# Performance work log

Measured on AMD Instinct MI355X. Metric: run time of the kernel, lower is better.

Reference implementation:

```python
import jax, jax.numpy as jnp
import numpy as np

B, T, TQ, E = 32, 200, 50, 64
P, C = 128, 64
BN_EPS = 1e-6
DICE_EPS = 1e-6


def _bn(x, g, b, m, v):
    # inference-mode batch norm over last axis
    return (x - m) * jax.lax.rsqrt(v + BN_EPS) * g + b


def _dice(x, alpha, m, v):
    # Dice activation: p = sigmoid(BN(x, no scale/shift)); out = p*x + alpha*(1-p)*x
    p = jax.nn.sigmoid((x - m) * jax.lax.rsqrt(v + DICE_EPS))
    return p * x + alpha * (1.0 - p) * x


def setup_inputs() -> dict:
    key = jax.random.key(0)
    ks = jax.random.split(key, 16)
    def g(k, shape, scale=0.05):
        return jax.random.normal(k, shape, dtype=jnp.float32) * scale
    inp = {
        "user_behavior": jax.random.normal(ks[0], (B, T, E), dtype=jnp.float32),
        "items": jax.random.normal(ks[1], (B, TQ, E), dtype=jnp.float32),
        "user_profile": jax.random.normal(ks[2], (B, P), dtype=jnp.float32),
        "context": jax.random.normal(ks[3], (B, C), dtype=jnp.float32),
        # attention MLP
        "W1": g(ks[4], (4 * E, 36)), "b1": jnp.zeros((36,), jnp.float32),
        "dice_alpha": jnp.zeros((36,), jnp.float32),
        "dice_mean": jnp.zeros((36,), jnp.float32),
        "dice_var": jnp.ones((36,), jnp.float32),
        "W2": g(ks[5], (36, 1)), "b2": jnp.zeros((1,), jnp.float32),
        # trunk MLP (input dim E+P+C = 256)
        "bn1_g": jnp.ones((E + P + C,), jnp.float32), "bn1_b": jnp.zeros((E + P + C,), jnp.float32),
        "bn1_m": jnp.zeros((E + P + C,), jnp.float32), "bn1_v": jnp.ones((E + P + C,), jnp.float32),
        "Wm1": g(ks[6], (E + P + C, 256)), "bm1": jnp.zeros((256,), jnp.float32),
        "bn2_g": jnp.ones((256,), jnp.float32), "bn2_b": jnp.zeros((256,), jnp.float32),
        "bn2_m": jnp.zeros((256,), jnp.float32), "bn2_v": jnp.ones((256,), jnp.float32),
        "Wm2": g(ks[7], (256, 128)), "bm2": jnp.zeros((128,), jnp.float32),
        "bn3_g": jnp.ones((128,), jnp.float32), "bn3_b": jnp.zeros((128,), jnp.float32),
        "bn3_m": jnp.zeros((128,), jnp.float32), "bn3_v": jnp.ones((128,), jnp.float32),
        "Wm3": g(ks[8], (128, 64)), "bm3": jnp.zeros((64,), jnp.float32),
    }
    return inp


def reference(user_behavior, items, user_profile, context,
              W1, b1, dice_alpha, dice_mean, dice_var, W2, b2,
              bn1_g, bn1_b, bn1_m, bn1_v, Wm1, bm1,
              bn2_g, bn2_b, bn2_m, bn2_v, Wm2, bm2,
              bn3_g, bn3_b, bn3_m, bn3_v, Wm3, bm3):
    b, t, e = user_behavior.shape
    tq = items.shape[1]
    # tile/concat cross product: (B, T', T, 4E)
    q = jnp.broadcast_to(user_behavior[:, None, :, :], (b, tq, t, e))
    k = jnp.broadcast_to(items[:, :, None, :], (b, tq, t, e))
    x = jnp.concatenate([q, k, q - k, q * k], axis=-1)
    x = jnp.einsum('btsf,fu->btsu', x, W1) + b1
    x = _dice(x, dice_alpha, dice_mean, dice_var)
    weight = (jnp.einsum('btsu,uo->btso', x, W2) + b2)[..., 0]  # (B, T', T)
    # weighted sum over history: (B, T', E)
    interest = jnp.einsum('bts,bse->bte', weight, user_behavior)
    # trunk MLP (dropout is identity at inference)
    up = jnp.broadcast_to(user_profile[:, None, :], (b, tq, user_profile.shape[-1]))
    cx = jnp.broadcast_to(context[:, None, :], (b, tq, context.shape[-1]))
    h = jnp.concatenate([interest, up, cx], axis=-1)
    h = _bn(h, bn1_g, bn1_b, bn1_m, bn1_v)
    h = jax.nn.relu(h @ Wm1 + bm1)
    h = _bn(h, bn2_g, bn2_b, bn2_m, bn2_v)
    h = jax.nn.relu(h @ Wm2 + bm2)
    h = _bn(h, bn3_g, bn3_b, bn3_m, bn3_v)
    h = jax.nn.relu(h @ Wm3 + bm3)
    return h
```

## Files before the change

kernel.cpp:

```cpp
#include <hip/hip_runtime.h>
#include <hip/hip_bf16.h>
#include <math.h>

#define NB  32
#define NT  200
#define NTQ 50
#define NE  64
#define NP  128
#define NC  64
#define NU  36
#define NROW (NB * NTQ)

typedef __attribute__((ext_vector_type(8))) short bf8;
typedef __attribute__((ext_vector_type(4))) float f4;

#define KW_F32   0
#define BF_BASE  57600
#define W1F_OFF  0
#define WM1F_OFF 6144
#define WM2F_OFF 71680
#define WM3F_OFF 104448
#define HH_OFF   112640

__device__ __forceinline__ short f2bf(float x) {
    __hip_bfloat16 h = __float2bfloat16(x);
    return __builtin_bit_cast(short, h);
}

__device__ __forceinline__ void pack_frag(int j, const float* W, int N, int ksc, short* dst) {
    int i    = j & 7;
    int lane = (j >> 3) & 63;
    int tile = j >> 9;
    int ks = tile % ksc;
    int nt = tile / ksc;
    int k = ks * 32 + 8 * (lane >> 4) + i;
    int n = nt * 16 + (lane & 15);
    dst[j] = f2bf(W[k * N + n]);
}

__global__ __launch_bounds__(256) void prep(
    const float* __restrict__ it,
    const float* __restrict__ up, const float* __restrict__ cx,
    const float* __restrict__ W1, const float* __restrict__ b1,
    const float* __restrict__ Wm1, const float* __restrict__ Wm2, const float* __restrict__ Wm3,
    const float* __restrict__ bn1_g, const float* __restrict__ bn1_b,
    const float* __restrict__ bn1_m, const float* __restrict__ bn1_v,
    float* __restrict__ kW,
    short* __restrict__ w1f, short* __restrict__ wm1f,
    short* __restrict__ wm2f, short* __restrict__ wm3f, short* __restrict__ Hh)
{
    int idx = blockIdx.x * 256 + threadIdx.x;
    if (idx < NB * NTQ * NU) {
        int u = idx % NU, row = idx / NU;
        const float* k = it + row * NE;
        float acc = b1[u];
        #pragma unroll 4
        for (int e = 0; e < NE; ++e)
            acc = fmaf(k[e], W1[(64 + e) * NU + u] - W1[(128 + e) * NU + u], acc);
        kW[idx] = acc;
        return;
    }
    idx -= NB * NTQ * NU;
    if (idx < 6144) {
        int i = idx & 7, lane = (idx >> 3) & 63, tile = idx >> 9;
        int ks = tile & 3, nt = tile >> 2;
        int kk = ks * 32 + 8 * (lane >> 4) + i;
        int n  = nt * 16 + (lane & 15);
        float v = 0.f;
        if (n < NU) {
            v = W1[(128 + kk) * NU + n];
            if (kk < 64) v += W1[kk * NU + n];
        }
        w1f[idx] = f2bf(v);
        return;
    }
    idx -= 6144;
    if (idx < 65536) { pack_frag(idx, Wm1, 256, 8, wm1f); return; }
    idx -= 65536;
    if (idx < 32768) { pack_frag(idx, Wm2, 128, 8, wm2f); return; }
    idx -= 32768;
    if (idx < 8192)  { pack_frag(idx, Wm3,  64, 4, wm3f); return; }
    idx -= 8192;
    if (idx < NROW * 192) {
        int row = idx / 192, c = idx % 192;
        int col = 64 + c, b = row / NTQ;
        float val = (c < NP) ? up[b * NP + c] : cx[b * NC + (c - NP)];
        float hn = (val - bn1_m[col]) * rsqrtf(bn1_v[col] + 1e-6f) * bn1_g[col] + bn1_b[col];
        Hh[row * 256 + col] = f2bf(hn);
    }
}

struct AParams {
    const float *ub, *it, *kW, *W2, *b2, *da, *dm, *dv;
    const float *bn1_g, *bn1_b, *bn1_m, *bn1_v;
    const short *w1f;
    short* Hh;
};

__global__ __launch_bounds__(256) void attn(AParams P) {
    __shared__ float w_s[NT];
    __shared__ float red_s[256];

    const int tid = threadIdx.x;
    const int l = tid & 63, w = tid >> 6;
    const int tq = blockIdx.x, b = blockIdx.y;

    bf8 bfr[3][4];
    {
        const bf8* wf = (const bf8*)P.w1f;
        #pragma unroll
        for (int nt = 0; nt < 3; ++nt)
            #pragma unroll
            for (int ks = 0; ks < 4; ++ks)
                bfr[nt][ks] = wf[(nt * 4 + ks) * 64 + l];
    }

    float itv[2][8];
    {
        const float* itr = P.it + ((size_t)b * NTQ + tq) * NE;
        #pragma unroll
        for (int ks = 0; ks < 2; ++ks) {
            int e0 = ks * 32 + 8 * (l >> 4);
            f4 v0 = *(const f4*)(itr + e0);
            f4 v1 = *(const f4*)(itr + e0 + 4);
            #pragma unroll
            for (int i = 0; i < 4; ++i) { itv[ks][i] = v0[i]; itv[ks][4 + i] = v1[i]; }
        }
    }

    const int ul = l & 15;
    float kwv[3], dmv[3], drs[3], dav[3], w2v[3];
    {
        const float* kwr = P.kW + ((size_t)b * NTQ + tq) * NU;
        #pragma unroll
        for (int nt = 0; nt < 3; ++nt) {
            int u = nt * 16 + ul;
            bool v = (u < NU);
            int uc = v ? u : (NU - 1);
            kwv[nt] = v ? kwr[uc] : 0.f;
            dmv[nt] = P.dm[uc];
            drs[nt] = rsqrtf(P.dv[uc] + 1e-6f);
            dav[nt] = P.da[uc];
            w2v[nt] = v ? P.W2[uc] : 0.f;
        }
    }
    const float b2s = P.b2[0];

    for (int tt = w; tt < 13; tt += 4) {
        const int t0 = tt * 16;
        const int tA = t0 + (l & 15);

        bf8 aq[2], ap[2];
        if (tA < NT) {
            const float* ubr = P.ub + ((size_t)b * NT + tA) * NE;
            #pragma unroll
            for (int ks = 0; ks < 2; ++ks) {
                int e0 = ks * 32 + 8 * (l >> 4);
                f4 u0 = *(const f4*)(ubr + e0);
                f4 u1 = *(const f4*)(ubr + e0 + 4);
                #pragma unroll
                for (int i = 0; i < 4; ++i) {
                    aq[ks][i]     = f2bf(u0[i]);
                    aq[ks][4 + i] = f2bf(u1[i]);
                    ap[ks][i]     = f2bf(u0[i] * itv[ks][i]);
                    ap[ks][4 + i] = f2bf(u1[i] * itv[ks][4 + i]);
                }
            }
        } else {
            #pragma unroll
            for (int ks = 0; ks < 2; ++ks)
                #pragma unroll
                for (int i = 0; i < 8; ++i) { aq[ks][i] = 0; ap[ks][i] = 0; }
        }

        f4 acc[3];
        #pragma unroll
        for (int nt = 0; nt < 3; ++nt) { acc[nt][0]=0.f; acc[nt][1]=0.f; acc[nt][2]=0.f; acc[nt][3]=0.f; }
        #pragma unroll
        for (int nt = 0; nt < 3; ++nt) {
            acc[nt] = __builtin_amdgcn_mfma_f32_16x16x32_bf16(aq[0], bfr[nt][0], acc[nt], 0, 0, 0);
            acc[nt] = __builtin_amdgcn_mfma_f32_16x16x32_bf16(aq[1], bfr[nt][1], acc[nt], 0, 0, 0);
            acc[nt] = __builtin_amdgcn_mfma_f32_16x16x32_bf16(ap[0], bfr[nt][2], acc[nt], 0, 0, 0);
            acc[nt] = __builtin_amdgcn_mfma_f32_16x16x32_bf16(ap[1], bfr[nt][3], acc[nt], 0, 0, 0);
        }

        const int tD = t0 + 4 * (l >> 4);
        #pragma unroll
        for (int i = 0; i < 4; ++i) {
            int t = tD + i;
            bool tv = (t < NT);
            float val = 0.f;
            #pragma unroll
            for (int nt = 0; nt < 3; ++nt) {
                float x = acc[nt][i] + kwv[nt];
                float z = (x - dmv[nt]) * drs[nt];
                float p = 1.f / (1.f + __expf(-z));
                val += x * (dav[nt] + p * (1.f - dav[nt])) * w2v[nt];
            }
            val += __shfl_xor(val, 1);
            val += __shfl_xor(val, 2);
            val += __shfl_xor(val, 4);
            val += __shfl_xor(val, 8);
            if (ul == 0 && tv) w_s[t] = val + b2s;
        }
    }
    __syncthreads();

    {
        const int e = tid & 63, g = tid >> 6;
        const float* ubb = P.ub + (size_t)b * NT * NE;
        float s = 0.f;
        #pragma unroll 5
        for (int t = g * 50; t < g * 50 + 50; ++t)
            s = fmaf(w_s[t], ubb[t * NE + e], s);
        red_s[tid] = s;
    }
    __syncthreads();
    if (tid < 64) {
        float tot = red_s[tid] + red_s[64 + tid] + red_s[128 + tid] + red_s[192 + tid];
        float hn = (tot - P.bn1_m[tid]) * rsqrtf(P.bn1_v[tid] + 1e-6f) * P.bn1_g[tid] + P.bn1_b[tid];
        P.Hh[((size_t)b * NTQ + tq) * 256 + tid] = f2bf(hn);
    }
}

struct TParams {
    const short *Hh, *wm1f, *wm2f, *wm3f;
    const float *bm1, *bm2, *bm3;
    const float *bn2_g, *bn2_b, *bn2_m, *bn2_v;
    const float *bn3_g, *bn3_b, *bn3_m, *bn3_v;
    float* out;
};

#define LSTR 264

__global__ __launch_bounds__(256) void trunk(TParams P) {
    __shared__ short Ha[32 * LSTR];
    __shared__ short Hb[32 * LSTR];

    const int tid = threadIdx.x;
    const int l = tid & 63, w = tid >> 6;
    const int mt = w & 1, nh = w >> 1;
    const int row0 = blockIdx.x * 32;

    {
        const bf8* src = (const bf8*)(P.Hh + (size_t)row0 * 256);
        for (int ch = tid; ch < 32 * 32; ch += 256) {
            int r = ch >> 5, c8 = ch & 31;
            *(bf8*)&Ha[r * LSTR + c8 * 8] = src[r * 32 + c8];
        }
    }
    __syncthreads();

    const int ar = mt * 16 + (l & 15);
    const int rl = mt * 16 + 4 * (l >> 4);
    const int nl = l & 15;

    {
        bf8 a[8];
        #pragma unroll
        for (int ks = 0; ks < 8; ++ks)
            a[ks] = *(const bf8*)&Ha[ar * LSTR + ks * 32 + 8 * (l >> 4)];
        const bf8* wf = (const bf8*)P.wm1f;
        #pragma unroll
        for (int nt0 = 0; nt0 < 8; ++nt0) {
            int nt = nh * 8 + nt0;
            f4 acc; acc[0]=0.f; acc[1]=0.f; acc[2]=0.f; acc[3]=0.f;
            #pragma unroll
            for (int ks = 0; ks < 8; ++ks)
                acc = __builtin_amdgcn_mfma_f32_16x16x32_bf16(a[ks], wf[(nt * 8 + ks) * 64 + l], acc, 0, 0, 0);
            int n = nt * 16 + nl;
            float g1 = P.bn2_g[n] * rsqrtf(P.bn2_v[n] + 1e-6f);
            float c1 = P.bn2_b[n] - P.bn2_m[n] * g1;
            float bias = P.bm1[n];
            #pragma unroll
            for (int i = 0; i < 4; ++i) {
                float v = fmaxf(acc[i] + bias, 0.f);
                Hb[(rl + i) * LSTR + n] = f2bf(v * g1 + c1);
            }
        }
    }
    __syncthreads();

    {
        bf8 a[8];
        #pragma unroll
        for (int ks = 0; ks < 8; ++ks)
            a[ks] = *(const bf8*)&Hb[ar * LSTR + ks * 32 + 8 * (l >> 4)];
        const bf8* wf = (const bf8*)P.wm2f;
        #pragma unroll
        for (int nt0 = 0; nt0 < 4; ++nt0) {
            int nt = nh * 4 + nt0;
            f4 acc; acc[0]=0.f; acc[1]=0.f; acc[2]=0.f; acc[3]=0.f;
            #pragma unroll
            for (int ks = 0; ks < 8; ++ks)
                acc = __builtin_amdgcn_mfma_f32_16x16x32_bf16(a[ks], wf[(nt * 8 + ks) * 64 + l], acc, 0, 0, 0);
            int n = nt * 16 + nl;
            float g1 = P.bn3_g[n] * rsqrtf(P.bn3_v[n] + 1e-6f);
            float c1 = P.bn3_b[n] - P.bn3_m[n] * g1;
            float bias = P.bm2[n];
            #pragma unroll
            for (int i = 0; i < 4; ++i) {
                float v = fmaxf(acc[i] + bias, 0.f);
                Ha[(rl + i) * LSTR + n] = f2bf(v * g1 + c1);
            }
        }
    }
    __syncthreads();

    {
        bf8 a[4];
        #pragma unroll
        for (int ks = 0; ks < 4; ++ks)
            a[ks] = *(const bf8*)&Ha[ar * LSTR + ks * 32 + 8 * (l >> 4)];
        const bf8* wf = (const bf8*)P.wm3f;
        #pragma unroll
        for (int nt0 = 0; nt0 < 2; ++nt0) {
            int nt = nh * 2 + nt0;
            f4 acc; acc[0]=0.f; acc[1]=0.f; acc[2]=0.f; acc[3]=0.f;
            #pragma unroll
            for (int ks = 0; ks < 4; ++ks)
                acc = __builtin_amdgcn_mfma_f32_16x16x32_bf16(a[ks], wf[(nt * 4 + ks) * 64 + l], acc, 0, 0, 0);
            int n = nt * 16 + nl;
            float bias = P.bm3[n];
            #pragma unroll
            for (int i = 0; i < 4; ++i)
                P.out[(size_t)(row0 + rl + i) * 64 + n] = fmaxf(acc[i] + bias, 0.f);
        }
    }
}

extern "C" void kernel_launch(void* const* d_in, const int* in_sizes, int n_in,
                              void* d_out, int out_size, void* d_ws, size_t ws_size,
                              hipStream_t stream) {
    (void)in_sizes; (void)n_in; (void)out_size; (void)ws_size;

    const float* ub         = (const float*)d_in[0];
    const float* it         = (const float*)d_in[1];
    const float* up         = (const float*)d_in[2];
    const float* cx         = (const float*)d_in[3];
    const float* W1         = (const float*)d_in[4];
    const float* b1         = (const float*)d_in[5];
    const float* dice_alpha = (const float*)d_in[6];
    const float* dice_mean  = (const float*)d_in[7];
    const float* dice_var   = (const float*)d_in[8];
    const float* W2         = (const float*)d_in[9];
    const float* b2         = (const float*)d_in[10];
    const float* bn1_g      = (const float*)d_in[11];
    const float* bn1_b      = (const float*)d_in[12];
    const float* bn1_m      = (const float*)d_in[13];
    const float* bn1_v      = (const float*)d_in[14];
    const float* Wm1        = (const float*)d_in[15];
    const float* bm1        = (const float*)d_in[16];
    const float* bn2_g      = (const float*)d_in[17];
    const float* bn2_b      = (const float*)d_in[18];
    const float* bn2_m      = (const float*)d_in[19];
    const float* bn2_v      = (const float*)d_in[20];
    const float* Wm2        = (const float*)d_in[21];
    const float* bm2        = (const float*)d_in[22];
    const float* bn3_g      = (const float*)d_in[23];
    const float* bn3_b      = (const float*)d_in[24];
    const float* bn3_m      = (const float*)d_in[25];
    const float* bn3_v      = (const float*)d_in[26];
    const float* Wm3        = (const float*)d_in[27];
    const float* bm3        = (const float*)d_in[28];

    float* kW  = (float*)d_ws + KW_F32;
    short* wsb = (short*)((float*)d_ws + BF_BASE);
    short* w1f  = wsb + W1F_OFF;
    short* wm1f = wsb + WM1F_OFF;
    short* wm2f = wsb + WM2F_OFF;
    short* wm3f = wsb + WM3F_OFF;
    short* Hh   = wsb + HH_OFF;

    const int prep_total = NB * NTQ * NU + 6144 + 65536 + 32768 + 8192 + NROW * 192;
    prep<<<(prep_total + 255) / 256, 256, 0, stream>>>(
        it, up, cx, W1, b1, Wm1, Wm2, Wm3,
        bn1_g, bn1_b, bn1_m, bn1_v,
        kW, w1f, wm1f, wm2f, wm3f, Hh);

    AParams A;
    A.ub = ub; A.it = it; A.kW = kW;
    A.W2 = W2; A.b2 = b2; A.da = dice_alpha; A.dm = dice_mean; A.dv = dice_var;
    A.bn1_g = bn1_g; A.bn1_b = bn1_b; A.bn1_m = bn1_m; A.bn1_v = bn1_v;
    A.w1f = w1f; A.Hh = Hh;
    attn<<<dim3(NTQ, NB), 256, 0, stream>>>(A);

    TParams T;
    T.Hh = Hh; T.wm1f = wm1f; T.wm2f = wm2f; T.wm3f = wm3f;
    T.bm1 = bm1; T.bm2 = bm2; T.bm3 = bm3;
    T.bn2_g = bn2_g; T.bn2_b = bn2_b; T.bn2_m = bn2_m; T.bn2_v = bn2_v;
    T.bn3_g = bn3_g; T.bn3_b = bn3_b; T.bn3_m = bn3_m; T.bn3_v = bn3_v;
    T.out = (float*)d_out;
    trunk<<<NROW / 32, 256, 0, stream>>>(T);
}
```

Before: 183.5 us.

## Fuse profile/context BN into trunk and halve trunk row tile to 16

```diff
diff --git a/kernel.cpp b/kernel.cpp
--- a/kernel.cpp
+++ b/kernel.cpp
@@ -40,14 +40,11 @@
 
 __global__ __launch_bounds__(256) void prep(
     const float* __restrict__ it,
-    const float* __restrict__ up, const float* __restrict__ cx,
     const float* __restrict__ W1, const float* __restrict__ b1,
     const float* __restrict__ Wm1, const float* __restrict__ Wm2, const float* __restrict__ Wm3,
-    const float* __restrict__ bn1_g, const float* __restrict__ bn1_b,
-    const float* __restrict__ bn1_m, const float* __restrict__ bn1_v,
     float* __restrict__ kW,
     short* __restrict__ w1f, short* __restrict__ wm1f,
-    short* __restrict__ wm2f, short* __restrict__ wm3f, short* __restrict__ Hh)
+    short* __restrict__ wm2f, short* __restrict__ wm3f)
 {
     int idx = blockIdx.x * 256 + threadIdx.x;
     if (idx < NB * NTQ * NU) {
@@ -80,14 +77,6 @@
     if (idx < 32768) { pack_frag(idx, Wm2, 128, 8, wm2f); return; }
     idx -= 32768;
     if (idx < 8192)  { pack_frag(idx, Wm3,  64, 4, wm3f); return; }
-    idx -= 8192;
-    if (idx < NROW * 192) {
-        int row = idx / 192, c = idx % 192;
-        int col = 64 + c, b = row / NTQ;
-        float val = (c < NP) ? up[b * NP + c] : cx[b * NC + (c - NP)];
-        float hn = (val - bn1_m[col]) * rsqrtf(bn1_v[col] + 1e-6f) * bn1_g[col] + bn1_b[col];
-        Hh[row * 256 + col] = f2bf(hn);
-    }
 }
 
 struct AParams {
@@ -219,12 +208,14 @@
     if (tid < 64) {
         float tot = red_s[tid] + red_s[64 + tid] + red_s[128 + tid] + red_s[192 + tid];
         float hn = (tot - P.bn1_m[tid]) * rsqrtf(P.bn1_v[tid] + 1e-6f) * P.bn1_g[tid] + P.bn1_b[tid];
-        P.Hh[((size_t)b * NTQ + tq) * 256 + tid] = f2bf(hn);
+        P.Hh[((size_t)b * NTQ + tq) * 64 + tid] = f2bf(hn);
     }
 }
 
 struct TParams {
     const short *Hh, *wm1f, *wm2f, *wm3f;
+    const float *up, *cx;
+    const float *bn1_g, *bn1_b, *bn1_m, *bn1_v;
     const float *bm1, *bm2, *bm3;
     const float *bn2_g, *bn2_b, *bn2_m, *bn2_v;
     const float *bn3_g, *bn3_b, *bn3_m, *bn3_v;
@@ -234,25 +225,33 @@
 #define LSTR 264
 
 __global__ __launch_bounds__(256) void trunk(TParams P) {
-    __shared__ short Ha[32 * LSTR];
-    __shared__ short Hb[32 * LSTR];
+    __shared__ short Ha[16 * LSTR];
+    __shared__ short Hb[16 * LSTR];
 
     const int tid = threadIdx.x;
     const int l = tid & 63, w = tid >> 6;
-    const int mt = w & 1, nh = w >> 1;
-    const int row0 = blockIdx.x * 32;
-
-    {
-        const bf8* src = (const bf8*)(P.Hh + (size_t)row0 * 256);
-        for (int ch = tid; ch < 32 * 32; ch += 256) {
-            int r = ch >> 5, c8 = ch & 31;
-            *(bf8*)&Ha[r * LSTR + c8 * 8] = src[r * 32 + c8];
-        }
-    }
-    __syncthreads();
-
-    const int ar = mt * 16 + (l & 15);
-    const int rl = mt * 16 + 4 * (l >> 4);
+    const int row0 = blockIdx.x * 16;
+
+    {
+        const bf8* src = (const bf8*)(P.Hh + (size_t)row0 * 64);
+        for (int ch = tid; ch < 16 * 8; ch += 256) {
+            int r = ch >> 3, c8 = ch & 7;
+            *(bf8*)&Ha[r * LSTR + c8 * 8] = src[r * 8 + c8];
+        }
+    }
+    for (int ch = tid; ch < 16 * 192; ch += 256) {
+        int r = ch / 192, c = ch % 192;
+        int col = 64 + c;
+        int b = (row0 + r) / NTQ;
+        float val = (c < NP) ? P.up[b * NP + c] : P.cx[b * NC + (c - NP)];
+        float hn = (val - P.bn1_m[col]) * rsqrtf(P.bn1_v[col] + 1e-6f)
+                   * P.bn1_g[col] + P.bn1_b[col];
+        Ha[r * LSTR + col] = f2bf(hn);
+    }
+    __syncthreads();
+
+    const int ar = l & 15;
+    const int rl = 4 * (l >> 4);
     const int nl = l & 15;
 
     {
@@ -262,8 +261,8 @@
             a[ks] = *(const bf8*)&Ha[ar * LSTR + ks * 32 + 8 * (l >> 4)];
         const bf8* wf = (const bf8*)P.wm1f;
         #pragma unroll
-        for (int nt0 = 0; nt0 < 8; ++nt0) {
-            int nt = nh * 8 + nt0;
+        for (int nt0 = 0; nt0 < 4; ++nt0) {
+            int nt = w * 4 + nt0;
             f4 acc; acc[0]=0.f; acc[1]=0.f; acc[2]=0.f; acc[3]=0.f;
             #pragma unroll
             for (int ks = 0; ks < 8; ++ks)
@@ -288,8 +287,8 @@
             a[ks] = *(const bf8*)&Hb[ar * LSTR + ks * 32 + 8 * (l >> 4)];
         const bf8* wf = (const bf8*)P.wm2f;
         #pragma unroll
-        for (int nt0 = 0; nt0 < 4; ++nt0) {
-            int nt = nh * 4 + nt0;
+        for (int nt0 = 0; nt0 < 2; ++nt0) {
+            int nt = w * 2 + nt0;
             f4 acc; acc[0]=0.f; acc[1]=0.f; acc[2]=0.f; acc[3]=0.f;
             #pragma unroll
             for (int ks = 0; ks < 8; ++ks)
@@ -313,9 +312,8 @@
         for (int ks = 0; ks < 4; ++ks)
             a[ks] = *(const bf8*)&Ha[ar * LSTR + ks * 32 + 8 * (l >> 4)];
         const bf8* wf = (const bf8*)P.wm3f;
-        #pragma unroll
-        for (int nt0 = 0; nt0 < 2; ++nt0) {
-            int nt = nh * 2 + nt0;
+        {
+            int nt = w;
             f4 acc; acc[0]=0.f; acc[1]=0.f; acc[2]=0.f; acc[3]=0.f;
             #pragma unroll
             for (int ks = 0; ks < 4; ++ks)
@@ -372,11 +370,10 @@
     short* wm3f = wsb + WM3F_OFF;
     short* Hh   = wsb + HH_OFF;
 
-    const int prep_total = NB * NTQ * NU + 6144 + 65536 + 32768 + 8192 + NROW * 192;
+    const int prep_total = NB * NTQ * NU + 6144 + 65536 + 32768 + 8192;
     prep<<<(prep_total + 255) / 256, 256, 0, stream>>>(
-        it, up, cx, W1, b1, Wm1, Wm2, Wm3,
-        bn1_g, bn1_b, bn1_m, bn1_v,
-        kW, w1f, wm1f, wm2f, wm3f, Hh);
+        it, W1, b1, Wm1, Wm2, Wm3,
+        kW, w1f, wm1f, wm2f, wm3f);
 
     AParams A;
     A.ub = ub; A.it = it; A.kW = kW;
@@ -387,9 +384,11 @@
 
     TParams T;
     T.Hh = Hh; T.wm1f = wm1f; T.wm2f = wm2f; T.wm3f = wm3f;
+    T.up = up; T.cx = cx;
+    T.bn1_g = bn1_g; T.bn1_b = bn1_b; T.bn1_m = bn1_m; T.bn1_v = bn1_v;
     T.bm1 = bm1; T.bm2 = bm2; T.bm3 = bm3;
     T.bn2_g = bn2_g; T.bn2_b = bn2_b; T.bn2_m = bn2_m; T.bn2_v = bn2_v;
     T.bn3_g = bn3_g; T.bn3_b = bn3_b; T.bn3_m = bn3_m; T.bn3_v = bn3_v;
     T.out = (float*)d_out;
-    trunk<<<NROW / 32, 256, 0, stream>>>(T);
-}
+    trunk<<<NROW / 16, 256, 0, stream>>>(T);
+}
```

Measured after the change: 153.1 us. 16.6% less time.
